# Kernel tuning notes

Hardware: AMD Instinct MI355X
Metric: run time of the kernel (lower is better)

The kernel has to match this reference:

```python
import jax, jax.numpy as jnp
import numpy as np

NEG_SLOPE = 0.2

def setup_inputs() -> dict:
    key = jax.random.key(0)
    k1, k2, k3, k4 = jax.random.split(key, 4)
    B, n, d_in, d_out = 8, 2048, 128, 128
    x = jax.random.normal(k1, (B, n, d_in), dtype=jnp.float32)
    adj = jax.random.uniform(k2, (B, n, n), dtype=jnp.float32)
    # glorot init for W: std = sqrt(2/(fan_in+fan_out))
    W = jax.random.normal(k3, (d_in, d_out), dtype=jnp.float32) * np.sqrt(2.0 / (d_in + d_out))
    a = jax.random.normal(k4, (2 * d_out,), dtype=jnp.float32) * np.sqrt(2.0 / (2 * d_out + 1))
    return {"x": x, "adj": adj, "W": W, "a": a}

def reference(x, adj, W, a):
    d_out = W.shape[1]
    h = jnp.einsum('bni,io->bno', x, W)               # [B,n,d_out]
    x_weighted = jnp.einsum('bnm,bmo->bno', adj, h)   # adj @ Wx
    # additive attention: a @ concat(h_i, h_j) == h_i@a_src + h_j@a_dst
    a_src, a_dst = a[:d_out], a[d_out:]
    s_i = h @ a_src                                   # [B,n]
    s_j = h @ a_dst                                   # [B,n]
    e = jax.nn.leaky_relu(s_i[:, :, None] + s_j[:, None, :], NEG_SLOPE)  # [B,n,n]
    alpha = jax.nn.softmax(e, axis=2)
    out = jnp.einsum('bnm,bmo->bno', alpha, h) + x_weighted
    return jax.nn.leaky_relu(out, NEG_SLOPE)
```

## Files before the change

### kernel.cpp

```cpp
#include <hip/hip_runtime.h>
#include <hip/hip_bf16.h>

#define NEG 0.2f
#define LOG2E 1.4426950408889634f

typedef __attribute__((ext_vector_type(8))) short bf16x8;
typedef __attribute__((ext_vector_type(4))) float f32x4;
typedef __attribute__((ext_vector_type(16))) float f32x16;
typedef __attribute__((ext_vector_type(4))) int int4v;

__device__ __forceinline__ float lrelu(float t){ return fmaxf(t, NEG * t); }
__device__ __forceinline__ float fast_exp2(float x){
  float r; asm("v_exp_f32 %0, %1" : "=v"(r) : "v"(x)); return r;
}
__device__ __forceinline__ unsigned short f2bf(float f){
  union { float f; unsigned int u; } v; v.f = f;
  unsigned int r = v.u + 0x7FFFu + ((v.u >> 16) & 1u);
  return (unsigned short)(r >> 16);
}
__device__ __forceinline__ unsigned fmap(float f){
  unsigned u = __float_as_uint(f);
  return (u & 0x80000000u) ? ~u : (u | 0x80000000u);
}
__device__ __forceinline__ float funmap(unsigned u){
  return (u & 0x80000000u) ? __uint_as_float(u & 0x7FFFFFFFu) : __uint_as_float(~u);
}

__global__ __launch_bounds__(256) void k0_wt(const float* __restrict__ W,
                                             unsigned short* __restrict__ Wt,
                                             unsigned* __restrict__ Mu){
  __shared__ __align__(16) unsigned short wl[8*136];
  const int t = threadIdx.x;
  const int p = blockIdx.x;
  if (p == 0 && t < 8) Mu[t] = 0u;
  {
    const int k = t >> 1, h = t & 1;
    f32x4 v = *(const f32x4*)(W + k*128 + p*8 + h*4);
#pragma unroll
    for (int e = 0; e < 4; ++e) wl[(h*4 + e)*136 + k] = f2bf(v[e]);
  }
  __syncthreads();
  {
    const int ol = t >> 5, ks = (t & 31) * 4;
    unsigned int lo = *(const unsigned int*)(wl + ol*136 + ks);
    unsigned int hi = *(const unsigned int*)(wl + ol*136 + ks + 2);
    *(unsigned int*)(Wt + (p*8 + ol)*128 + ks)     = lo;
    *(unsigned int*)(Wt + (p*8 + ol)*128 + ks + 2) = hi;
  }
}

__global__ __launch_bounds__(256) void k1_fused(const float* __restrict__ x,
                                                const unsigned short* __restrict__ Wt,
                                                const float* __restrict__ a,
                                                unsigned short* __restrict__ ht,
                                                float* __restrict__ ssrcL,
                                                float* __restrict__ sdstL,
                                                unsigned* __restrict__ Mu){
  __shared__ __align__(16) unsigned short wtl[128*136];
  __shared__ __align__(16) unsigned short xl[32*136];
  __shared__ __align__(16) unsigned short tlw[128*34];
  __shared__ float sred[2][4][2][16];
  const int t = threadIdx.x;
  const int bx = blockIdx.x;
  const int b  = bx >> 6;
  const int jt = bx & 63;
  const long rowbase = (long)bx * 32;
  {
    const int o = t >> 1, seg = (t & 1) * 64;
    const int4v* src = (const int4v*)(Wt + o*128 + seg);
    int4v* dst = (int4v*)(wtl + o*136 + seg);
#pragma unroll
    for (int g = 0; g < 8; ++g) dst[g] = src[g];
  }
  {
    const int i = t >> 3, ks = (t & 7) * 16;
    const f32x4* src = (const f32x4*)(x + (rowbase + i)*128 + ks);
    unsigned int q[8];
#pragma unroll
    for (int g = 0; g < 4; ++g){
      f32x4 v = src[g];
      q[g*2]   = (unsigned)f2bf(v[0]) | ((unsigned)f2bf(v[1]) << 16);
      q[g*2+1] = (unsigned)f2bf(v[2]) | ((unsigned)f2bf(v[3]) << 16);
    }
    int4v* dst = (int4v*)(xl + i*136 + ks);
    dst[0] = *(int4v*)&q[0];
    dst[1] = *(int4v*)&q[4];
  }
  __syncthreads();
  const int w = t >> 6, lane = t & 63, lr = lane & 15, hi = lane >> 4;
  f32x4 zro = {0.f, 0.f, 0.f, 0.f};
  f32x4 acc00 = zro, acc01 = zro, acc10 = zro, acc11 = zro;
#pragma unroll
  for (int ks = 0; ks < 4; ++ks){
    const bf16x8 a0 = *(const bf16x8*)(wtl + (w*32      + lr)*136 + ks*32 + hi*8);
    const bf16x8 a1 = *(const bf16x8*)(wtl + (w*32 + 16 + lr)*136 + ks*32 + hi*8);
    const bf16x8 b0 = *(const bf16x8*)(xl + (     lr)*136 + ks*32 + hi*8);
    const bf16x8 b1 = *(const bf16x8*)(xl + (16 + lr)*136 + ks*32 + hi*8);
    acc00 = __builtin_amdgcn_mfma_f32_16x16x32_bf16(a0, b0, acc00, 0, 0, 0);
    acc01 = __builtin_amdgcn_mfma_f32_16x16x32_bf16(a0, b1, acc01, 0, 0, 0);
    acc10 = __builtin_amdgcn_mfma_f32_16x16x32_bf16(a1, b0, acc10, 0, 0, 0);
    acc11 = __builtin_amdgcn_mfma_f32_16x16x32_bf16(a1, b1, acc11, 0, 0, 0);
  }
  {
    const f32x4 as0 = *(const f32x4*)(a +       w*32      + hi*4);
    const f32x4 as1 = *(const f32x4*)(a +       w*32 + 16 + hi*4);
    const f32x4 ad0 = *(const f32x4*)(a + 128 + w*32      + hi*4);
    const f32x4 ad1 = *(const f32x4*)(a + 128 + w*32 + 16 + hi*4);
    float ps0, ps1, pd0, pd1;
    {
      f32x4 u = acc00*as0 + acc10*as1;  ps0 = u[0]+u[1]+u[2]+u[3];
      f32x4 v = acc01*as0 + acc11*as1;  ps1 = v[0]+v[1]+v[2]+v[3];
      f32x4 p = acc00*ad0 + acc10*ad1;  pd0 = p[0]+p[1]+p[2]+p[3];
      f32x4 r = acc01*ad0 + acc11*ad1;  pd1 = r[0]+r[1]+r[2]+r[3];
    }
#pragma unroll
    for (int off = 16; off <= 32; off <<= 1){
      ps0 += __shfl_xor(ps0, off); ps1 += __shfl_xor(ps1, off);
      pd0 += __shfl_xor(pd0, off); pd1 += __shfl_xor(pd1, off);
    }
    if (hi == 0){
      sred[0][w][0][lr] = ps0; sred[0][w][1][lr] = ps1;
      sred[1][w][0][lr] = pd0; sred[1][w][1][lr] = pd1;
    }
  }
#pragma unroll
  for (int q = 0; q < 4; ++q){
    tlw[(w*32      + hi*4 + q)*34      + lr] = f2bf(acc00[q]);
    tlw[(w*32      + hi*4 + q)*34 + 16 + lr] = f2bf(acc01[q]);
    tlw[(w*32 + 16 + hi*4 + q)*34      + lr] = f2bf(acc10[q]);
    tlw[(w*32 + 16 + hi*4 + q)*34 + 16 + lr] = f2bf(acc11[q]);
  }
  __syncthreads();
  {
    const int o = t >> 1, jseg = (t & 1) * 16;
    const unsigned int* src = (const unsigned int*)(tlw + o*34 + jseg);
    unsigned int p[8];
#pragma unroll
    for (int g = 0; g < 8; ++g) p[g] = src[g];
    unsigned short* dst = ht + (long)b*262144 + (long)o*2048 + jt*32 + jseg;
    ((int4v*)dst)[0] = *(int4v*)&p[0];
    ((int4v*)dst)[1] = *(int4v*)&p[4];
  }
  if (t < 64){
    const int sel = t >> 5, jl = t & 31;
    const int ig = jl >> 4, l2 = jl & 15;
    const float s = (sred[sel][0][ig][l2] + sred[sel][1][ig][l2]
                   + sred[sel][2][ig][l2] + sred[sel][3][ig][l2]) * LOG2E;
    if (sel == 0){
      ssrcL[rowbase + jl] = s;
    } else {
      sdstL[rowbase + jl] = s;
      unsigned u = fmap(s);
#pragma unroll
      for (int off = 1; off <= 16; off <<= 1){
        unsigned o2 = (unsigned)__shfl_xor((int)u, off);
        u = u > o2 ? u : o2;
      }
      if (jl == 0) atomicMax(&Mu[b], u);
    }
  }
}

__global__ __launch_bounds__(256) void k2_ml(const float* __restrict__ ssrcL,
                                             const float* __restrict__ sdstL,
                                             const unsigned* __restrict__ Mu,
                                             float* __restrict__ carr){
  const int lane = threadIdx.x & 63;
  const long row = (long)blockIdx.x * 4 + (threadIdx.x >> 6);
  const int b = (int)(row >> 11);
  const float siL = ssrcL[row];
  const float mL = lrelu(siL + funmap(Mu[b]));
  const float* sd = sdstL + (long)b*2048;
  float sum = 0.f;
#pragma unroll
  for (int k = 0; k < 8; ++k){
    f32x4 v = *(const f32x4*)(sd + lane*4 + k*256);
#pragma unroll
    for (int e = 0; e < 4; ++e) sum += fast_exp2(lrelu(siL + v[e]) - mL);
  }
#pragma unroll
  for (int off = 1; off <= 32; off <<= 1) sum += __shfl_xor(sum, off);
  if (lane == 0) carr[row] = mL + __log2f(sum);
}

__global__ __launch_bounds__(256, 2) void k3_main(const float* __restrict__ adj,
                                                  const unsigned short* __restrict__ ht,
                                                  const float* __restrict__ ssrcL,
                                                  const float* __restrict__ sdstL,
                                                  const float* __restrict__ carr,
                                                  float* __restrict__ out){
  __shared__ __align__(16) unsigned short httile[2][128][64];
  __shared__ __align__(16) unsigned short wtile[2][32][64];
  const int t    = threadIdx.x;
  const int bxr  = blockIdx.x;
  const int bx   = ((bxr & 7) << 6) | (bxr >> 3);
  const int b    = bx >> 6;
  const int i0   = (bx & 63) * 32;
  const int w    = t >> 6, lane = t & 63;
  const int r32  = lane & 31, hl = lane >> 5;
  const int r7   = r32 & 7;
  const int wchunk = (w*2 + hl) ^ r7;
  const long rowg = (long)b*2048 + i0 + r32;
  const float siL = ssrcL[rowg];
  const float Ci  = carr[rowg];
  const float* adjL = adj + rowg*2048 + w*16 + hl*8;
  const float* sdbL = sdstL + (long)b*2048 + w*16 + hl*8;
  const unsigned short* sgbase = ht + (long)b*262144
                               + (long)(w*32 + (lane >> 3))*2048
                               + ((lane & 7) ^ (lane >> 3)) * 8;

  f32x16 acc;
#pragma unroll
  for (int e = 0; e < 16; ++e) acc[e] = 0.f;
  f32x4 aA0, aA1, dA0, dA1, aB0, aB1, dB0, dB1;

#pragma unroll
  for (int it = 0; it < 4; ++it)
    __builtin_amdgcn_global_load_lds(
      (const __attribute__((address_space(1))) void*)(sgbase + it*16384),
      (__attribute__((address_space(3))) void*)&httile[0][w*32 + it*8][0], 16, 0, 0);
  aA0 = *(const f32x4*)(adjL);      aA1 = *(const f32x4*)(adjL + 4);
  dA0 = *(const f32x4*)(sdbL);      dA1 = *(const f32x4*)(sdbL + 4);
  aB0 = *(const f32x4*)(adjL + 64); aB1 = *(const f32x4*)(adjL + 68);
  dB0 = *(const f32x4*)(sdbL + 64); dB1 = *(const f32x4*)(sdbL + 68);

#define K3_STEP(JB, BUF, DO_STAGE, DO_REFILL, VMSTR, AV0, AV1, DV0, DV1) do{     \
    if (DO_STAGE){                                                               \
      _Pragma("unroll")                                                          \
      for (int it = 0; it < 4; ++it)                                             \
        __builtin_amdgcn_global_load_lds(                                        \
          (const __attribute__((address_space(1))) void*)(sgbase + (JB) + 64 + it*16384), \
          (__attribute__((address_space(3))) void*)&httile[(BUF)^1][w*32 + it*8][0], 16, 0, 0); \
    }                                                                            \
    {  float wv[8];                                                              \
       _Pragma("unroll")                                                         \
       for (int e = 0; e < 4; ++e){                                              \
         wv[e]   = AV0[e] + fast_exp2(lrelu(siL + DV0[e]) - Ci);                 \
         wv[4+e] = AV1[e] + fast_exp2(lrelu(siL + DV1[e]) - Ci);                 \
       }                                                                         \
       const unsigned p01 = __builtin_amdgcn_perm(__float_as_uint(wv[1]), __float_as_uint(wv[0]), 0x07060302u); \
       const unsigned p23 = __builtin_amdgcn_perm(__float_as_uint(wv[3]), __float_as_uint(wv[2]), 0x07060302u); \
       const unsigned p45 = __builtin_amdgcn_perm(__float_as_uint(wv[5]), __float_as_uint(wv[4]), 0x07060302u); \
       const unsigned p67 = __builtin_amdgcn_perm(__float_as_uint(wv[7]), __float_as_uint(wv[6]), 0x07060302u); \
       int4v ai = {(int)p01, (int)p23, (int)p45, (int)p67};                      \
       *(int4v*)&wtile[BUF][r32][wchunk*8] = ai;                                 \
    }                                                                            \
    if (DO_REFILL){                                                              \
      AV0 = *(const f32x4*)(adjL + (JB) + 128);                                  \
      AV1 = *(const f32x4*)(adjL + (JB) + 132);                                  \
      DV0 = *(const f32x4*)(sdbL + (JB) + 128);                                  \
      DV1 = *(const f32x4*)(sdbL + (JB) + 132);                                  \
    }                                                                            \
    asm volatile("s_waitcnt vmcnt(" VMSTR ") lgkmcnt(0)" ::: "memory");          \
    __builtin_amdgcn_sched_barrier(0);                                           \
    __builtin_amdgcn_s_barrier();                                                \
    __builtin_amdgcn_sched_barrier(0);                                           \
    __builtin_amdgcn_s_setprio(1);                                               \
    _Pragma("unroll")                                                            \
    for (int g = 0; g < 4; ++g){                                                 \
      const int pos = ((2*g + hl) ^ r7) * 8;                                     \
      const bf16x8 afr = *(const bf16x8*)&wtile[BUF][r32][pos];                  \
      const bf16x8 bfr = *(const bf16x8*)&httile[BUF][w*32 + r32][pos];          \
      acc = __builtin_amdgcn_mfma_f32_32x32x16_bf16(afr, bfr, acc, 0, 0, 0);     \
    }                                                                            \
    __builtin_amdgcn_s_setprio(0);                                               \
    __builtin_amdgcn_sched_barrier(0);                                           \
  }while(0)

  for (int kt = 0; kt < 30; kt += 2){
    const int jb0 = kt * 64;
    K3_STEP(jb0,      0, 1, 1, "8", aA0, aA1, dA0, dA1);
    K3_STEP(jb0 + 64, 1, 1, 1, "8", aB0, aB1, dB0, dB1);
  }
  K3_STEP(1920, 0, 1, 0, "8", aA0, aA1, dA0, dA1);
  K3_STEP(1984, 1, 0, 0, "0", aB0, aB1, dB0, dB1);
#undef K3_STEP

#pragma unroll
  for (int rg = 0; rg < 16; ++rg){
    const int rr = (rg & 3) + 8*(rg >> 2) + 4*hl;
    out[((long)b*2048 + i0 + rr)*128 + w*32 + r32] = lrelu(acc[rg]);
  }
}

extern "C" void kernel_launch(void* const* d_in, const int* in_sizes, int n_in,
                              void* d_out, int out_size, void* d_ws, size_t ws_size,
                              hipStream_t stream){
  const float* x   = (const float*)d_in[0];
  const float* adj = (const float*)d_in[1];
  const float* W   = (const float*)d_in[2];
  const float* a   = (const float*)d_in[3];
  float* out = (float*)d_out;
  char* ws = (char*)d_ws;

  unsigned short* ht    = (unsigned short*)(ws);
  float*          ssrcL = (float*)(ws + 4194304);
  float*          sdstL = (float*)(ws + 4259840);
  float*          carr  = (float*)(ws + 4325376);
  unsigned short* Wt    = (unsigned short*)(ws + 4390912);
  unsigned*       Mu    = (unsigned*)(ws + 4423680);

  k0_wt   <<<16,   256, 0, stream>>>(W, Wt, Mu);
  k1_fused<<<512,  256, 0, stream>>>(x, Wt, a, ht, ssrcL, sdstL, Mu);
  k2_ml   <<<4096, 256, 0, stream>>>(ssrcL, sdstL, Mu, carr);
  k3_main <<<512,  256, 0, stream>>>(adj, ht, ssrcL, sdstL, carr, out);
}
```

Measured before the change: 57.39 us.

## Fuse softmax normalizer into main kernel using separate P and adj accumulators

```diff
diff --git a/kernel.cpp b/kernel.cpp
--- a/kernel.cpp
+++ b/kernel.cpp
@@ -161,36 +161,17 @@
   }
 }
 
-__global__ __launch_bounds__(256) void k2_ml(const float* __restrict__ ssrcL,
-                                             const float* __restrict__ sdstL,
-                                             const unsigned* __restrict__ Mu,
-                                             float* __restrict__ carr){
-  const int lane = threadIdx.x & 63;
-  const long row = (long)blockIdx.x * 4 + (threadIdx.x >> 6);
-  const int b = (int)(row >> 11);
-  const float siL = ssrcL[row];
-  const float mL = lrelu(siL + funmap(Mu[b]));
-  const float* sd = sdstL + (long)b*2048;
-  float sum = 0.f;
-#pragma unroll
-  for (int k = 0; k < 8; ++k){
-    f32x4 v = *(const f32x4*)(sd + lane*4 + k*256);
-#pragma unroll
-    for (int e = 0; e < 4; ++e) sum += fast_exp2(lrelu(siL + v[e]) - mL);
-  }
-#pragma unroll
-  for (int off = 1; off <= 32; off <<= 1) sum += __shfl_xor(sum, off);
-  if (lane == 0) carr[row] = mL + __log2f(sum);
-}
-
 __global__ __launch_bounds__(256, 2) void k3_main(const float* __restrict__ adj,
                                                   const unsigned short* __restrict__ ht,
                                                   const float* __restrict__ ssrcL,
                                                   const float* __restrict__ sdstL,
-                                                  const float* __restrict__ carr,
+                                                  const unsigned* __restrict__ Mu,
                                                   float* __restrict__ out){
   __shared__ __align__(16) unsigned short httile[2][128][64];
-  __shared__ __align__(16) unsigned short wtile[2][32][64];
+  __shared__ __align__(16) unsigned short atile[2][32][64];
+  __shared__ __align__(16) unsigned short ptile[2][32][64];
+  __shared__ float lred[32][8];
+  __shared__ float linv[32];
   const int t    = threadIdx.x;
   const int bxr  = blockIdx.x;
   const int bx   = ((bxr & 7) << 6) | (bxr >> 3);
@@ -202,16 +183,17 @@
   const int wchunk = (w*2 + hl) ^ r7;
   const long rowg = (long)b*2048 + i0 + r32;
   const float siL = ssrcL[rowg];
-  const float Ci  = carr[rowg];
+  const float mL  = lrelu(siL + funmap(Mu[b]));
   const float* adjL = adj + rowg*2048 + w*16 + hl*8;
   const float* sdbL = sdstL + (long)b*2048 + w*16 + hl*8;
   const unsigned short* sgbase = ht + (long)b*262144
                                + (long)(w*32 + (lane >> 3))*2048
                                + ((lane & 7) ^ (lane >> 3)) * 8;
 
-  f32x16 acc;
-#pragma unroll
-  for (int e = 0; e < 16; ++e) acc[e] = 0.f;
+  f32x16 acc_a, acc_p;
+#pragma unroll
+  for (int e = 0; e < 16; ++e){ acc_a[e] = 0.f; acc_p[e] = 0.f; }
+  float lsum = 0.f;
   f32x4 aA0, aA1, dA0, dA1, aB0, aB1, dB0, dB1;
 
 #pragma unroll
@@ -232,18 +214,25 @@
           (const __attribute__((address_space(1))) void*)(sgbase + (JB) + 64 + it*16384), \
           (__attribute__((address_space(3))) void*)&httile[(BUF)^1][w*32 + it*8][0], 16, 0, 0); \
     }                                                                            \
-    {  float wv[8];                                                              \
+    {  float pv[8];                                                              \
        _Pragma("unroll")                                                         \
        for (int e = 0; e < 4; ++e){                                              \
-         wv[e]   = AV0[e] + fast_exp2(lrelu(siL + DV0[e]) - Ci);                 \
-         wv[4+e] = AV1[e] + fast_exp2(lrelu(siL + DV1[e]) - Ci);                 \
+         pv[e]   = fast_exp2(lrelu(siL + DV0[e]) - mL);                          \
+         pv[4+e] = fast_exp2(lrelu(siL + DV1[e]) - mL);                          \
        }                                                                         \
-       const unsigned p01 = __builtin_amdgcn_perm(__float_as_uint(wv[1]), __float_as_uint(wv[0]), 0x07060302u); \
-       const unsigned p23 = __builtin_amdgcn_perm(__float_as_uint(wv[3]), __float_as_uint(wv[2]), 0x07060302u); \
-       const unsigned p45 = __builtin_amdgcn_perm(__float_as_uint(wv[5]), __float_as_uint(wv[4]), 0x07060302u); \
-       const unsigned p67 = __builtin_amdgcn_perm(__float_as_uint(wv[7]), __float_as_uint(wv[6]), 0x07060302u); \
-       int4v ai = {(int)p01, (int)p23, (int)p45, (int)p67};                      \
-       *(int4v*)&wtile[BUF][r32][wchunk*8] = ai;                                 \
+       lsum += ((pv[0]+pv[1])+(pv[2]+pv[3])) + ((pv[4]+pv[5])+(pv[6]+pv[7]));    \
+       const unsigned q01 = __builtin_amdgcn_perm(__float_as_uint(pv[1]), __float_as_uint(pv[0]), 0x07060302u); \
+       const unsigned q23 = __builtin_amdgcn_perm(__float_as_uint(pv[3]), __float_as_uint(pv[2]), 0x07060302u); \
+       const unsigned q45 = __builtin_amdgcn_perm(__float_as_uint(pv[5]), __float_as_uint(pv[4]), 0x07060302u); \
+       const unsigned q67 = __builtin_amdgcn_perm(__float_as_uint(pv[7]), __float_as_uint(pv[6]), 0x07060302u); \
+       int4v pi = {(int)q01, (int)q23, (int)q45, (int)q67};                      \
+       *(int4v*)&ptile[BUF][r32][wchunk*8] = pi;                                 \
+       const unsigned a01 = __builtin_amdgcn_perm(__float_as_uint(AV0[1]), __float_as_uint(AV0[0]), 0x07060302u); \
+       const unsigned a23 = __builtin_amdgcn_perm(__float_as_uint(AV0[3]), __float_as_uint(AV0[2]), 0x07060302u); \
+       const unsigned a45 = __builtin_amdgcn_perm(__float_as_uint(AV1[1]), __float_as_uint(AV1[0]), 0x07060302u); \
+       const unsigned a67 = __builtin_amdgcn_perm(__float_as_uint(AV1[3]), __float_as_uint(AV1[2]), 0x07060302u); \
+       int4v ai = {(int)a01, (int)a23, (int)a45, (int)a67};                      \
+       *(int4v*)&atile[BUF][r32][wchunk*8] = ai;                                 \
     }                                                                            \
     if (DO_REFILL){                                                              \
       AV0 = *(const f32x4*)(adjL + (JB) + 128);                                  \
@@ -259,9 +248,11 @@
     _Pragma("unroll")                                                            \
     for (int g = 0; g < 4; ++g){                                                 \
       const int pos = ((2*g + hl) ^ r7) * 8;                                     \
-      const bf16x8 afr = *(const bf16x8*)&wtile[BUF][r32][pos];                  \
       const bf16x8 bfr = *(const bf16x8*)&httile[BUF][w*32 + r32][pos];          \
-      acc = __builtin_amdgcn_mfma_f32_32x32x16_bf16(afr, bfr, acc, 0, 0, 0);     \
+      const bf16x8 afr = *(const bf16x8*)&atile[BUF][r32][pos];                  \
+      const bf16x8 pfr = *(const bf16x8*)&ptile[BUF][r32][pos];                  \
+      acc_a = __builtin_amdgcn_mfma_f32_32x32x16_bf16(afr, bfr, acc_a, 0, 0, 0); \
+      acc_p = __builtin_amdgcn_mfma_f32_32x32x16_bf16(pfr, bfr, acc_p, 0, 0, 0); \
     }                                                                            \
     __builtin_amdgcn_s_setprio(0);                                               \
     __builtin_amdgcn_sched_barrier(0);                                           \
@@ -276,10 +267,19 @@
   K3_STEP(1984, 1, 0, 0, "0", aB0, aB1, dB0, dB1);
 #undef K3_STEP
 
+  lred[r32][w*2 + hl] = lsum;
+  __syncthreads();
+  if (t < 32){
+    const float* lr = &lred[t][0];
+    const float l = ((lr[0]+lr[1]) + (lr[2]+lr[3])) + ((lr[4]+lr[5]) + (lr[6]+lr[7]));
+    linv[t] = 1.f / l;
+  }
+  __syncthreads();
 #pragma unroll
   for (int rg = 0; rg < 16; ++rg){
     const int rr = (rg & 3) + 8*(rg >> 2) + 4*hl;
-    out[((long)b*2048 + i0 + rr)*128 + w*32 + r32] = lrelu(acc[rg]);
+    const float v = acc_a[rg] + acc_p[rg] * linv[rr];
+    out[((long)b*2048 + i0 + rr)*128 + w*32 + r32] = lrelu(v);
   }
 }
 
@@ -296,12 +296,10 @@
   unsigned short* ht    = (unsigned short*)(ws);
   float*          ssrcL = (float*)(ws + 4194304);
   float*          sdstL = (float*)(ws + 4259840);
-  float*          carr  = (float*)(ws + 4325376);
-  unsigned short* Wt    = (unsigned short*)(ws + 4390912);
-  unsigned*       Mu    = (unsigned*)(ws + 4423680);
-
-  k0_wt   <<<16,   256, 0, stream>>>(W, Wt, Mu);
-  k1_fused<<<512,  256, 0, stream>>>(x, Wt, a, ht, ssrcL, sdstL, Mu);
-  k2_ml   <<<4096, 256, 0, stream>>>(ssrcL, sdstL, Mu, carr);
-  k3_main <<<512,  256, 0, stream>>>(adj, ht, ssrcL, sdstL, carr, out);
-}
+  unsigned short* Wt    = (unsigned short*)(ws + 4325376);
+  unsigned*       Mu    = (unsigned*)(ws + 4358144);
+
+  k0_wt   <<<16,  256, 0, stream>>>(W, Wt, Mu);
+  k1_fused<<<512, 256, 0, stream>>>(x, Wt, a, ht, ssrcL, sdstL, Mu);
+  k3_main <<<512, 256, 0, stream>>>(adj, ht, ssrcL, sdstL, Mu, out);
+}
```

Result: faster. 53.00 us (-7.7%).
